# Performance work log

Hardware: AMD Instinct MI355X
Metric: run time of the kernel (lower is better)

## Reference

```python
import jax, jax.numpy as jnp
import numpy as np

LATENT = 1024
HIDDEN = 1024
VOCAB = 32000
SEQ = 129      # y_len
STRIDE = 128   # number of decode steps = y_len - 1


def setup_inputs() -> dict:
    key = jax.random.key(0)
    ks = jax.random.split(key, 16)
    s = 0.05  # weight scale to keep gates in a sane range
    H, L, V = HIDDEN, LATENT, VOCAB
    return {
        "y": jax.random.randint(ks[0], (SEQ,), 0, V),
        "context_vector": jax.random.normal(ks[1], (2, L), jnp.float32),
        "stride": STRIDE,
        # fc_upscale: latent -> hidden
        "W_up": jax.random.normal(ks[2], (H, L), jnp.float32) * s,
        "b_up": jax.random.normal(ks[3], (H,), jnp.float32) * s,
        # LSTM layer 0 (input_size = 1), torch gate order [i, f, g, o]
        "W_ih0": jax.random.normal(ks[4], (4 * H, 1), jnp.float32) * s,
        "W_hh0": jax.random.normal(ks[5], (4 * H, H), jnp.float32) * s,
        "b_ih0": jax.random.normal(ks[6], (4 * H,), jnp.float32) * s,
        "b_hh0": jax.random.normal(ks[7], (4 * H,), jnp.float32) * s,
        # LSTM layer 1 (input_size = hidden)
        "W_ih1": jax.random.normal(ks[8], (4 * H, H), jnp.float32) * s,
        "W_hh1": jax.random.normal(ks[9], (4 * H, H), jnp.float32) * s,
        "b_ih1": jax.random.normal(ks[10], (4 * H,), jnp.float32) * s,
        "b_hh1": jax.random.normal(ks[11], (4 * H,), jnp.float32) * s,
        # fc_out: hidden -> vocab
        "W_out": jax.random.normal(ks[12], (V, H), jnp.float32) * s,
        "b_out": jax.random.normal(ks[13], (V,), jnp.float32) * s,
    }


def _lstm_cell(x, h, c, Wi, Wh, bi, bh):
    # torch nn.LSTM gate layout: [input, forget, cell(g), output]
    g = Wi @ x + bi + Wh @ h + bh          # [4H]
    i, f, gg, o = jnp.split(g, 4)
    i = jax.nn.sigmoid(i)
    f = jax.nn.sigmoid(f)
    gg = jnp.tanh(gg)
    o = jax.nn.sigmoid(o)
    c2 = f * c + i * gg
    return o * jnp.tanh(c2), c2


def reference(y, context_vector, stride, W_up, b_up,
              W_ih0, W_hh0, b_ih0, b_hh0,
              W_ih1, W_hh1, b_ih1, b_hh1,
              W_out, b_out):
    # non-bidirectional path: ctx = ctx[0] * ctx[1]; both layers share the
    # same upscaled context for h0 and c0 (torch.cat([ctx]*num_layers)).
    ctx = context_vector[0] * context_vector[1]       # [latent]
    h_init = W_up @ ctx + b_up                        # [hidden]
    tok0 = y[0].astype(jnp.float32)

    def step(carry, _):
        h0, c0, h1, c1, tok = carry
        x = tok[None]                                  # [1] LSTM input (token id as float)
        h0, c0 = _lstm_cell(x, h0, c0, W_ih0, W_hh0, b_ih0, b_hh0)
        h1, c1 = _lstm_cell(h0, h1, c1, W_ih1, W_hh1, b_ih1, b_hh1)
        preds = jax.nn.relu(W_out @ h1 + b_out)        # [vocab]
        nxt = jax.lax.stop_gradient(jnp.argmax(preds)).astype(jnp.float32)
        return (h0, c0, h1, c1, nxt), preds

    init = (h_init, h_init, h_init, h_init, tok0)
    _, outputs = jax.lax.scan(step, init, None, length=int(stride))  # [stride, vocab]
    # eval mode: log_softmax over vocab
    return jax.nn.log_softmax(outputs, axis=1)
```

## Files before the change

kernel.cpp:

```cpp
#include <hip/hip_runtime.h>

#define H 1024
#define V 32000
#define NSTEP 128
#define LBLK 1000
#define LROWS 32
#define LTHR 512
#define NBLK_L 256
#define NTHR_L 512

#define WS_G0    0
#define WS_HINIT 8192
#define WS_C0    9216
#define WS_H1    11264
#define WS_C1    13312
#define WS_PMAX  14336
#define WS_PIDX  16384

__device__ __forceinline__ float sigmoidf_(float x) { return 1.f / (1.f + expf(-x)); }

__device__ __forceinline__ float wred(float a) {
#pragma unroll
    for (int o = 32; o > 0; o >>= 1) a += __shfl_down(a, o, 64);
    return a;
}

__device__ __forceinline__ float dot_row(const float4* __restrict__ w4,
                                         const float4* h, int lane) {
    float a = 0.f;
#pragma unroll
    for (int k = 0; k < 4; ++k) {
        float4 w = w4[lane + (k << 6)];
        a += w.x * h[k].x + w.y * h[k].y + w.z * h[k].z + w.w * h[k].w;
    }
    return a;
}

__global__ __launch_bounds__(256) void k_setup(const float* __restrict__ Wup,
                                               const float* __restrict__ bup,
                                               const float* __restrict__ cv,
                                               float* __restrict__ ws) {
    int r = blockIdx.x, t = threadIdx.x;
    __shared__ float red[256];
    const float* row = Wup + (size_t)r * H;
    float acc = 0.f;
    for (int j = t; j < H; j += 256) acc += row[j] * (cv[j] * cv[H + j]);
    red[t] = acc;
    __syncthreads();
    for (int s = 128; s > 0; s >>= 1) { if (t < s) red[t] += red[t + s]; __syncthreads(); }
    if (t == 0) {
        float h = red[0] + bup[r];
        ws[WS_HINIT + r] = h;
        ws[WS_C0 + r] = h;
        ws[WS_H1 + r] = h;
        ws[WS_C1 + r] = h;
    }
}

__global__ __launch_bounds__(256) void k_g0(const float* __restrict__ Whh0,
                                            const float* __restrict__ bih0,
                                            const float* __restrict__ bhh0,
                                            float* __restrict__ ws) {
    int b = blockIdx.x, t = threadIdx.x;
    int w = t >> 6, lane = t & 63;
    float4 hreg[4];
#pragma unroll
    for (int k = 0; k < 4; ++k) hreg[k] = ((const float4*)(ws + WS_HINIT))[lane + (k << 6)];
    int r = (b << 2) + w;
    float a = wred(dot_row((const float4*)(Whh0 + (size_t)r * H), hreg, lane));
    if (lane == 0) ws[WS_G0 + r] = a + bih0[r] + bhh0[r];
}

__global__ __launch_bounds__(NTHR_L) void k_L(
    const int* __restrict__ y,
    const float* __restrict__ Wih0col,
    const float* __restrict__ Whh0,
    const float* __restrict__ bih0, const float* __restrict__ bhh0,
    const float* __restrict__ Wih1, const float* __restrict__ Whh1,
    const float* __restrict__ bih1, const float* __restrict__ bhh1,
    float* __restrict__ ws, int step)
{
    const int b = blockIdx.x, t = threadIdx.x;
    const int w = t >> 6, lane = t & 63;
    const int p = step & 1;
    __shared__ float h0s[H];
    __shared__ float rm[NTHR_L];
    __shared__ int   ri[NTHR_L];
    __shared__ float gl[4][4];

    float tok;
    if (step == 0) {
        tok = (float)y[0];
    } else {
        float m = -1e30f;
        int idx = 0x7fffffff;
        for (int i = t; i < LBLK; i += NTHR_L) {
            float m2 = ws[WS_PMAX + i];
            int i2 = ((const int*)ws)[WS_PIDX + i];
            if (m2 > m) { m = m2; idx = i2; }
            else if (m2 == m && i2 < idx) idx = i2;
        }
        rm[t] = m; ri[t] = idx;
        __syncthreads();
        for (int o = NTHR_L >> 1; o > 0; o >>= 1) {
            if (t < o) {
                float m2 = rm[t + o]; int i2 = ri[t + o];
                if (m2 > rm[t]) { rm[t] = m2; ri[t] = i2; }
                else if (m2 == rm[t] && i2 < ri[t]) ri[t] = i2;
            }
            __syncthreads();
        }
        tok = (float)ri[0];
    }

    for (int c = t; c < H; c += NTHR_L) {
        float gi = ws[WS_G0 + p * 4096 + c]        + Wih0col[c]        * tok;
        float gf = ws[WS_G0 + p * 4096 + 1024 + c] + Wih0col[1024 + c] * tok;
        float gg = ws[WS_G0 + p * 4096 + 2048 + c] + Wih0col[2048 + c] * tok;
        float go = ws[WS_G0 + p * 4096 + 3072 + c] + Wih0col[3072 + c] * tok;
        float cc = sigmoidf_(gf) * ws[WS_C0 + p * H + c] + sigmoidf_(gi) * tanhf(gg);
        ws[WS_C0 + (p ^ 1) * H + c] = cc;
        h0s[c] = sigmoidf_(go) * tanhf(cc);
    }
    __syncthreads();

    float4 hx[4], hh[4];
#pragma unroll
    for (int k = 0; k < 4; ++k) {
        hx[k] = ((const float4*)h0s)[lane + (k << 6)];
        hh[k] = ((const float4*)(ws + WS_H1 + p * H))[lane + (k << 6)];
    }
    {
        const int cell = (b << 2) + (w >> 1);
        const int r0 = cell + ((w & 1) << 11);
        const int r1 = r0 + 1024;
        float a0 = dot_row((const float4*)(Wih1 + (size_t)r0 * H), hx, lane)
                 + dot_row((const float4*)(Whh1 + (size_t)r0 * H), hh, lane);
        float a1 = dot_row((const float4*)(Wih1 + (size_t)r1 * H), hx, lane)
                 + dot_row((const float4*)(Whh1 + (size_t)r1 * H), hh, lane);
        a0 = wred(a0); a1 = wred(a1);
        if (lane == 0) {
            int gi = (w & 1) << 1;
            gl[w >> 1][gi]     = a0 + bih1[r0] + bhh1[r0];
            gl[w >> 1][gi + 1] = a1 + bih1[r1] + bhh1[r1];
        }
    }
    {
        const int g0r = (b << 4) + (w << 1);
        float b0 = dot_row((const float4*)(Whh0 + (size_t)g0r * H), hx, lane);
        float b1 = dot_row((const float4*)(Whh0 + (size_t)(g0r + 1) * H), hx, lane);
        b0 = wred(b0); b1 = wred(b1);
        if (lane == 0) {
            ws[WS_G0 + (p ^ 1) * 4096 + g0r]     = b0 + bih0[g0r] + bhh0[g0r];
            ws[WS_G0 + (p ^ 1) * 4096 + g0r + 1] = b1 + bih0[g0r + 1] + bhh0[g0r + 1];
        }
    }
    __syncthreads();
    if (t < 4) {
        int cell = (b << 2) + t;
        float ig = sigmoidf_(gl[t][0]);
        float fg = sigmoidf_(gl[t][1]);
        float gg = tanhf(gl[t][2]);
        float og = sigmoidf_(gl[t][3]);
        float cc = fg * ws[WS_C1 + cell] + ig * gg;
        ws[WS_C1 + cell] = cc;
        ws[WS_H1 + (p ^ 1) * H + cell] = og * tanhf(cc);
    }
}

__global__ __launch_bounds__(LTHR) void k_logits(const float* __restrict__ Wout,
                                                 const float* __restrict__ bout,
                                                 float* __restrict__ outrow,
                                                 float* __restrict__ ws, int par) {
    __shared__ float pm[8];
    __shared__ int   pix[8];
    int b = blockIdx.x, t = threadIdx.x;
    int w = t >> 6, lane = t & 63;
    float4 hreg[4];
#pragma unroll
    for (int k = 0; k < 4; ++k)
        hreg[k] = ((const float4*)(ws + WS_H1 + par * H))[lane + (k << 6)];
    float m = -1e30f;
    int mi = 0x7fffffff;
    const int rbase = b * LROWS + (w << 2);
#pragma unroll
    for (int rr = 0; rr < 4; rr += 2) {
        int r = rbase + rr;
        float a0 = dot_row((const float4*)(Wout + (size_t)r * H), hreg, lane);
        float a1 = dot_row((const float4*)(Wout + (size_t)(r + 1) * H), hreg, lane);
        a0 = wred(a0); a1 = wred(a1);
        if (lane == 0) {
            float v0 = fmaxf(a0 + bout[r], 0.f);
            float v1 = fmaxf(a1 + bout[r + 1], 0.f);
            outrow[r] = v0; outrow[r + 1] = v1;
            if (v0 > m) { m = v0; mi = r; }
            if (v1 > m) { m = v1; mi = r + 1; }
        }
    }
    if (lane == 0) { pm[w] = m; pix[w] = mi; }
    __syncthreads();
    if (t == 0) {
        float bm = pm[0]; int bi = pix[0];
#pragma unroll
        for (int k = 1; k < 8; ++k) {
            if (pm[k] > bm) { bm = pm[k]; bi = pix[k]; }
            else if (pm[k] == bm && pix[k] < bi) bi = pix[k];
        }
        ws[WS_PMAX + b] = bm;
        ((int*)ws)[WS_PIDX + b] = bi;
    }
}

__global__ __launch_bounds__(1024) void k_final(float* __restrict__ out) {
    __shared__ float rm[1024], rs[1024];
    int s = blockIdx.x, t = threadIdx.x;
    float* row = out + (size_t)s * V;
    float m = -1e30f, sum = 0.f;
    for (int i = t; i < V; i += 1024) {
        float v = row[i];
        if (v > m) { sum = sum * expf(m - v) + 1.f; m = v; }
        else         sum += expf(v - m);
    }
    rm[t] = m; rs[t] = sum;
    __syncthreads();
    for (int o = 512; o > 0; o >>= 1) {
        if (t < o) {
            float m2 = rm[t + o], s2 = rs[t + o];
            if (m2 > rm[t]) { rs[t] = rs[t] * expf(rm[t] - m2) + s2; rm[t] = m2; }
            else              rs[t] += s2 * expf(m2 - rm[t]);
        }
        __syncthreads();
    }
    float logz = rm[0] + logf(rs[0]);
    for (int i = t; i < V; i += 1024) row[i] -= logz;
}

extern "C" void kernel_launch(void* const* d_in, const int* in_sizes, int n_in,
                              void* d_out, int out_size, void* d_ws, size_t ws_size,
                              hipStream_t stream) {
    const int*   y    = (const int*)d_in[0];
    const float* cv   = (const float*)d_in[1];
    const float* Wup  = (const float*)d_in[3];
    const float* bup  = (const float*)d_in[4];
    const float* Wih0 = (const float*)d_in[5];
    const float* Whh0 = (const float*)d_in[6];
    const float* bih0 = (const float*)d_in[7];
    const float* bhh0 = (const float*)d_in[8];
    const float* Wih1 = (const float*)d_in[9];
    const float* Whh1 = (const float*)d_in[10];
    const float* bih1 = (const float*)d_in[11];
    const float* bhh1 = (const float*)d_in[12];
    const float* Wout = (const float*)d_in[13];
    const float* bout = (const float*)d_in[14];
    float* out = (float*)d_out;
    float* ws  = (float*)d_ws;

    k_setup<<<1024, 256, 0, stream>>>(Wup, bup, cv, ws);
    k_g0<<<1024, 256, 0, stream>>>(Whh0, bih0, bhh0, ws);
    for (int t = 0; t < NSTEP; ++t) {
        k_L<<<NBLK_L, NTHR_L, 0, stream>>>(y, Wih0, Whh0, bih0, bhh0,
                                           Wih1, Whh1, bih1, bhh1, ws, t);
        k_logits<<<LBLK, LTHR, 0, stream>>>(Wout, bout, out + (size_t)t * V, ws, (t & 1) ^ 1);
    }
    k_final<<<NSTEP, 1024, 0, stream>>>(out);
}
```

Measured before the change: 4.763 ms.

## Use bf16 copy of output projection with fp32 rescue for close argmax

Converts W_out to bf16 once per call into the workspace and runs the per-step vocab projection from the bf16 copy, halving the weight bytes streamed each step. Blocks now track their top-2 logits; the next LSTM step merges them into a global top-3 and, when the top two are within a threshold, recomputes those candidates in fp32 so the chosen token matches the exact argmax. The logits written to the output are still computed from bf16 weights, so log_softmax values carry bf16 rounding error. If the workspace is too small, an fp32 fallback path is used.

Result: slower. 6.881 ms (+44.5%).

```diff
diff --git a/kernel.cpp b/kernel.cpp
--- a/kernel.cpp
+++ b/kernel.cpp
@@ -8,14 +8,19 @@
 #define LTHR 512
 #define NBLK_L 256
 #define NTHR_L 512
+#define RESCUE_TAU 0.1f
 
 #define WS_G0    0
 #define WS_HINIT 8192
 #define WS_C0    9216
 #define WS_H1    11264
 #define WS_C1    13312
-#define WS_PMAX  14336
-#define WS_PIDX  16384
+#define WS_PM1   14336
+#define WS_PIX1  16384
+#define WS_PM2   18432
+#define WS_PIX2  20480
+#define WS_WBF   24576
+#define WS_BF_BYTES_NEEDED ((size_t)(WS_WBF + 16384000) * 4)
 
 __device__ __forceinline__ float sigmoidf_(float x) { return 1.f / (1.f + expf(-x)); }
 
@@ -34,6 +39,39 @@
         a += w.x * h[k].x + w.y * h[k].y + w.z * h[k].z + w.w * h[k].w;
     }
     return a;
+}
+
+__device__ __forceinline__ unsigned bf16rne(float f) {
+    unsigned u = __float_as_uint(f);
+    return (u + 0x7FFFu + ((u >> 16) & 1u)) >> 16;
+}
+__device__ __forceinline__ unsigned pack2(float a, float b) {
+    return bf16rne(a) | (bf16rne(b) << 16);
+}
+__device__ __forceinline__ float bl(unsigned u) { return __uint_as_float(u << 16); }
+__device__ __forceinline__ float bh(unsigned u) { return __uint_as_float(u & 0xffff0000u); }
+
+__device__ __forceinline__ float dotbf(const uint4& qa, const uint4& qb,
+                                       const float4& ha, const float4& hb,
+                                       const float4& hc, const float4& hd) {
+    float a = 0.f;
+    a += bl(qa.x)*ha.x + bh(qa.x)*ha.y + bl(qa.y)*ha.z + bh(qa.y)*ha.w;
+    a += bl(qa.z)*hb.x + bh(qa.z)*hb.y + bl(qa.w)*hb.z + bh(qa.w)*hb.w;
+    a += bl(qb.x)*hc.x + bh(qb.x)*hc.y + bl(qb.y)*hc.z + bh(qb.y)*hc.w;
+    a += bl(qb.z)*hd.x + bh(qb.z)*hd.y + bl(qb.w)*hd.z + bh(qb.w)*hd.w;
+    return a;
+}
+
+__device__ __forceinline__ void upd2(float v, int r, float& m1, int& i1,
+                                     float& m2, int& i2) {
+    if (v > m1 || (v == m1 && r < i1)) { m2 = m1; i2 = i1; m1 = v; i1 = r; }
+    else if (v > m2 || (v == m2 && r < i2)) { m2 = v; i2 = r; }
+}
+__device__ __forceinline__ void upd3(float v, int r, float& m1, int& i1,
+                                     float& m2, int& i2, float& m3, int& i3) {
+    if (v > m1 || (v == m1 && r < i1)) { m3 = m2; i3 = i2; m2 = m1; i2 = i1; m1 = v; i1 = r; }
+    else if (v > m2 || (v == m2 && r < i2)) { m3 = m2; i3 = i2; m2 = v; i2 = r; }
+    else if (v > m3 || (v == m3 && r < i3)) { m3 = v; i3 = r; }
 }
 
 __global__ __launch_bounds__(256) void k_setup(const float* __restrict__ Wup,
@@ -71,6 +109,22 @@
     if (lane == 0) ws[WS_G0 + r] = a + bih0[r] + bhh0[r];
 }
 
+__global__ __launch_bounds__(256) void k_convert(const float* __restrict__ Wout,
+                                                 float* __restrict__ ws) {
+    uint4* dst = (uint4*)(ws + WS_WBF);
+    const int gid = blockIdx.x * 256 + threadIdx.x;
+    const int nth = gridDim.x * 256;
+    const int nchunk = (V * H) / 8;
+    for (int c = gid; c < nchunk; c += nth) {
+        float4 f0 = ((const float4*)Wout)[2 * c];
+        float4 f1 = ((const float4*)Wout)[2 * c + 1];
+        uint4 o;
+        o.x = pack2(f0.x, f0.y); o.y = pack2(f0.z, f0.w);
+        o.z = pack2(f1.x, f1.y); o.w = pack2(f1.z, f1.w);
+        dst[c] = o;
+    }
+}
+
 __global__ __launch_bounds__(NTHR_L) void k_L(
     const int* __restrict__ y,
     const float* __restrict__ Wih0col,
@@ -78,39 +132,73 @@
     const float* __restrict__ bih0, const float* __restrict__ bhh0,
     const float* __restrict__ Wih1, const float* __restrict__ Whh1,
     const float* __restrict__ bih1, const float* __restrict__ bhh1,
+    const float* __restrict__ WoutF, const float* __restrict__ bout,
     float* __restrict__ ws, int step)
 {
     const int b = blockIdx.x, t = threadIdx.x;
     const int w = t >> 6, lane = t & 63;
     const int p = step & 1;
     __shared__ float h0s[H];
-    __shared__ float rm[NTHR_L];
-    __shared__ int   ri[NTHR_L];
+    __shared__ float s1v[NTHR_L], s2v[NTHR_L], s3v[NTHR_L];
+    __shared__ int   s1i[NTHR_L], s2i[NTHR_L], s3i[NTHR_L];
     __shared__ float gl[4][4];
+    __shared__ float rv[3];
+    __shared__ int   rj[3];
 
     float tok;
     if (step == 0) {
         tok = (float)y[0];
     } else {
-        float m = -1e30f;
-        int idx = 0x7fffffff;
+        float a1 = -1e30f, a2 = -1e30f, a3 = -1e30f;
+        int j1 = 0x7fffffff, j2 = 0x7fffffff, j3 = 0x7fffffff;
         for (int i = t; i < LBLK; i += NTHR_L) {
-            float m2 = ws[WS_PMAX + i];
-            int i2 = ((const int*)ws)[WS_PIDX + i];
-            if (m2 > m) { m = m2; idx = i2; }
-            else if (m2 == m && i2 < idx) idx = i2;
-        }
-        rm[t] = m; ri[t] = idx;
+            upd3(ws[WS_PM1 + i], ((const int*)ws)[WS_PIX1 + i], a1, j1, a2, j2, a3, j3);
+            upd3(ws[WS_PM2 + i], ((const int*)ws)[WS_PIX2 + i], a1, j1, a2, j2, a3, j3);
+        }
+        s1v[t] = a1; s1i[t] = j1; s2v[t] = a2; s2i[t] = j2; s3v[t] = a3; s3i[t] = j3;
         __syncthreads();
         for (int o = NTHR_L >> 1; o > 0; o >>= 1) {
             if (t < o) {
-                float m2 = rm[t + o]; int i2 = ri[t + o];
-                if (m2 > rm[t]) { rm[t] = m2; ri[t] = i2; }
-                else if (m2 == rm[t] && i2 < ri[t]) ri[t] = i2;
+                float c1 = s1v[t], c2 = s2v[t], c3 = s3v[t];
+                int   d1 = s1i[t], d2 = s2i[t], d3 = s3i[t];
+                upd3(s1v[t + o], s1i[t + o], c1, d1, c2, d2, c3, d3);
+                upd3(s2v[t + o], s2i[t + o], c1, d1, c2, d2, c3, d3);
+                upd3(s3v[t + o], s3i[t + o], c1, d1, c2, d2, c3, d3);
+                s1v[t] = c1; s1i[t] = d1; s2v[t] = c2; s2i[t] = d2; s3v[t] = c3; s3i[t] = d3;
             }
             __syncthreads();
         }
-        tok = (float)ri[0];
+        float g1 = s1v[0], g2 = s2v[0];
+        int   c1 = s1i[0], c2 = s2i[0], c3 = s3i[0];
+        if (g1 - g2 < RESCUE_TAU) {
+            if (w < 3) {
+                int r = (w == 0) ? c1 : ((w == 1) ? c2 : c3);
+                float val = -1e30f;
+                if (r != 0x7fffffff) {
+                    const float4* wr = (const float4*)(WoutF + (size_t)r * H);
+                    const float4* h4 = (const float4*)(ws + WS_H1 + p * H);
+                    float d = 0.f;
+#pragma unroll
+                    for (int k = 0; k < 4; ++k) {
+                        float4 wv = wr[lane + (k << 6)];
+                        float4 hv = h4[lane + (k << 6)];
+                        d += wv.x * hv.x + wv.y * hv.y + wv.z * hv.z + wv.w * hv.w;
+                    }
+                    d = wred(d);
+                    val = fmaxf(d + bout[r], 0.f);
+                }
+                if (lane == 0) { rv[w] = val; rj[w] = r; }
+            }
+            __syncthreads();
+            float bv = rv[0]; int bj = rj[0];
+#pragma unroll
+            for (int k = 1; k < 3; ++k)
+                if (rv[k] > bv || (rv[k] == bv && rj[k] < bj)) { bv = rv[k]; bj = rj[k]; }
+            tok = (float)bj;
+        } else {
+            tok = (float)c1;
+        }
+        __syncthreads();
     }
 
     for (int c = t; c < H; c += NTHR_L) {
@@ -168,46 +256,92 @@
     }
 }
 
-__global__ __launch_bounds__(LTHR) void k_logits(const float* __restrict__ Wout,
-                                                 const float* __restrict__ bout,
-                                                 float* __restrict__ outrow,
-                                                 float* __restrict__ ws, int par) {
-    __shared__ float pm[8];
-    __shared__ int   pix[8];
+__global__ __launch_bounds__(LTHR) void k_logits_bf(const float* __restrict__ bout,
+                                                    float* __restrict__ outrow,
+                                                    float* __restrict__ ws, int par) {
+    __shared__ float wm1[8], wm2[8];
+    __shared__ int   wi1[8], wi2[8];
     int b = blockIdx.x, t = threadIdx.x;
     int w = t >> 6, lane = t & 63;
-    float4 hreg[4];
-#pragma unroll
-    for (int k = 0; k < 4; ++k)
-        hreg[k] = ((const float4*)(ws + WS_H1 + par * H))[lane + (k << 6)];
-    float m = -1e30f;
-    int mi = 0x7fffffff;
+    const float4* h4 = (const float4*)(ws + WS_H1 + par * H);
+    float4 ha = h4[2 * lane], hb = h4[2 * lane + 1];
+    float4 hc = h4[2 * lane + 128], hd = h4[2 * lane + 129];
+    const uint4* wb = (const uint4*)(ws + WS_WBF);
+    float m1 = -1e30f, m2 = -1e30f;
+    int i1 = 0x7fffffff, i2 = 0x7fffffff;
     const int rbase = b * LROWS + (w << 2);
 #pragma unroll
     for (int rr = 0; rr < 4; rr += 2) {
         int r = rbase + rr;
-        float a0 = dot_row((const float4*)(Wout + (size_t)r * H), hreg, lane);
-        float a1 = dot_row((const float4*)(Wout + (size_t)(r + 1) * H), hreg, lane);
-        a0 = wred(a0); a1 = wred(a1);
+        const uint4* r0p = wb + (size_t)r * 128;
+        const uint4* r1p = wb + (size_t)(r + 1) * 128;
+        uint4 qa0 = r0p[lane], qb0 = r0p[lane + 64];
+        uint4 qa1 = r1p[lane], qb1 = r1p[lane + 64];
+        float a0 = wred(dotbf(qa0, qb0, ha, hb, hc, hd));
+        float a1 = wred(dotbf(qa1, qb1, ha, hb, hc, hd));
         if (lane == 0) {
             float v0 = fmaxf(a0 + bout[r], 0.f);
             float v1 = fmaxf(a1 + bout[r + 1], 0.f);
             outrow[r] = v0; outrow[r + 1] = v1;
-            if (v0 > m) { m = v0; mi = r; }
-            if (v1 > m) { m = v1; mi = r + 1; }
-        }
-    }
-    if (lane == 0) { pm[w] = m; pix[w] = mi; }
+            upd2(v0, r, m1, i1, m2, i2);
+            upd2(v1, r + 1, m1, i1, m2, i2);
+        }
+    }
+    if (lane == 0) { wm1[w] = m1; wi1[w] = i1; wm2[w] = m2; wi2[w] = i2; }
     __syncthreads();
     if (t == 0) {
-        float bm = pm[0]; int bi = pix[0];
-#pragma unroll
-        for (int k = 1; k < 8; ++k) {
-            if (pm[k] > bm) { bm = pm[k]; bi = pix[k]; }
-            else if (pm[k] == bm && pix[k] < bi) bi = pix[k];
-        }
-        ws[WS_PMAX + b] = bm;
-        ((int*)ws)[WS_PIDX + b] = bi;
+        float g1 = -1e30f, g2 = -1e30f;
+        int j1 = 0x7fffffff, j2 = 0x7fffffff;
+#pragma unroll
+        for (int k = 0; k < 8; ++k) {
+            upd2(wm1[k], wi1[k], g1, j1, g2, j2);
+            upd2(wm2[k], wi2[k], g1, j1, g2, j2);
+        }
+        ws[WS_PM1 + b] = g1; ((int*)ws)[WS_PIX1 + b] = j1;
+        ws[WS_PM2 + b] = g2; ((int*)ws)[WS_PIX2 + b] = j2;
+    }
+}
+
+__global__ __launch_bounds__(LTHR) void k_logits_f32(const float* __restrict__ Wout,
+                                                     const float* __restrict__ bout,
+                                                     float* __restrict__ outrow,
+                                                     float* __restrict__ ws, int par) {
+    __shared__ float wm1[8], wm2[8];
+    __shared__ int   wi1[8], wi2[8];
+    int b = blockIdx.x, t = threadIdx.x;
+    int w = t >> 6, lane = t & 63;
+    float4 hreg[4];
+#pragma unroll
+    for (int k = 0; k < 4; ++k)
+        hreg[k] = ((const float4*)(ws + WS_H1 + par * H))[lane + (k << 6)];
+    float m1 = -1e30f, m2 = -1e30f;
+    int i1 = 0x7fffffff, i2 = 0x7fffffff;
+    const int rbase = b * LROWS + (w << 2);
+#pragma unroll
+    for (int rr = 0; rr < 4; rr += 2) {
+        int r = rbase + rr;
+        float a0 = wred(dot_row((const float4*)(Wout + (size_t)r * H), hreg, lane));
+        float a1 = wred(dot_row((const float4*)(Wout + (size_t)(r + 1) * H), hreg, lane));
+        if (lane == 0) {
+            float v0 = fmaxf(a0 + bout[r], 0.f);
+            float v1 = fmaxf(a1 + bout[r + 1], 0.f);
+            outrow[r] = v0; outrow[r + 1] = v1;
+            upd2(v0, r, m1, i1, m2, i2);
+            upd2(v1, r + 1, m1, i1, m2, i2);
+        }
+    }
+    if (lane == 0) { wm1[w] = m1; wi1[w] = i1; wm2[w] = m2; wi2[w] = i2; }
+    __syncthreads();
+    if (t == 0) {
+        float g1 = -1e30f, g2 = -1e30f;
+        int j1 = 0x7fffffff, j2 = 0x7fffffff;
+#pragma unroll
+        for (int k = 0; k < 8; ++k) {
+            upd2(wm1[k], wi1[k], g1, j1, g2, j2);
+            upd2(wm2[k], wi2[k], g1, j1, g2, j2);
+        }
+        ws[WS_PM1 + b] = g1; ((int*)ws)[WS_PIX1 + b] = j1;
+        ws[WS_PM2 + b] = g2; ((int*)ws)[WS_PIX2 + b] = j2;
     }
 }
 
@@ -255,12 +389,19 @@
     float* out = (float*)d_out;
     float* ws  = (float*)d_ws;
 
+    const bool bf = (ws_size >= WS_BF_BYTES_NEEDED);
+
     k_setup<<<1024, 256, 0, stream>>>(Wup, bup, cv, ws);
     k_g0<<<1024, 256, 0, stream>>>(Whh0, bih0, bhh0, ws);
+    if (bf) k_convert<<<2048, 256, 0, stream>>>(Wout, ws);
     for (int t = 0; t < NSTEP; ++t) {
         k_L<<<NBLK_L, NTHR_L, 0, stream>>>(y, Wih0, Whh0, bih0, bhh0,
-                                           Wih1, Whh1, bih1, bhh1, ws, t);
-        k_logits<<<LBLK, LTHR, 0, stream>>>(Wout, bout, out + (size_t)t * V, ws, (t & 1) ^ 1);
+                                           Wih1, Whh1, bih1, bhh1,
+                                           Wout, bout, ws, t);
+        if (bf)
+            k_logits_bf<<<LBLK, LTHR, 0, stream>>>(bout, out + (size_t)t * V, ws, (t & 1) ^ 1);
+        else
+            k_logits_f32<<<LBLK, LTHR, 0, stream>>>(Wout, bout, out + (size_t)t * V, ws, (t & 1) ^ 1);
     }
     k_final<<<NSTEP, 1024, 0, stream>>>(out);
 }
```
